# Kernel tuning notes

Hardware: AMD Instinct MI355X
Metric: run time of the kernel (lower is better)

The kernel has to match this reference:

```python
import jax, jax.numpy as jnp
import numpy as np

N_NODES = 50000
N_EDGES = 800000
IN_DIM = 128
HID = 128
NUM_GRAPHS = 64


def setup_inputs() -> dict:
    key = jax.random.key(0)
    ks = jax.random.split(key, 10)
    x = jax.random.normal(ks[0], (N_NODES, IN_DIM), dtype=jnp.float32)
    edge_index = jax.random.randint(ks[1], (2, N_EDGES), 0, N_NODES, dtype=jnp.int64)
    batch = jnp.sort(jax.random.randint(ks[2], (N_NODES,), 0, NUM_GRAPHS, dtype=jnp.int64))
    s = 1.0 / np.sqrt(IN_DIM)
    W0 = jax.random.uniform(ks[3], (IN_DIM, HID), jnp.float32, -s, s)
    b0 = jnp.zeros((HID,), jnp.float32)
    s = 1.0 / np.sqrt(HID)
    W1 = jax.random.uniform(ks[4], (HID, HID), jnp.float32, -s, s)
    b1 = jnp.zeros((HID,), jnp.float32)
    W2 = jax.random.uniform(ks[5], (HID, HID), jnp.float32, -s, s)
    b2 = jnp.zeros((HID,), jnp.float32)
    return {"x": x, "edge_index": edge_index, "batch": batch,
            "W0": W0, "b0": b0, "W1": W1, "b1": b1, "W2": W2, "b2": b2}


def reference(x, edge_index, batch, W0, b0, W1, b1, W2, b2):
    N = x.shape[0]
    # GCNConv: add self loops, symmetric degree normalization
    loop = jnp.arange(N, dtype=edge_index.dtype)
    src = jnp.concatenate([edge_index[0], loop])  # [E+N]
    dst = jnp.concatenate([edge_index[1], loop])
    deg = jax.ops.segment_sum(jnp.ones_like(dst, dtype=x.dtype), dst, num_segments=N)
    dinv = jnp.where(deg > 0, jax.lax.rsqrt(deg), 0.0)
    norm = (dinv[src] * dinv[dst])[:, None]  # [E+N, 1]

    def gcn_layer(h, W, b):
        h = h @ W  # [N, hid]
        agg = jax.ops.segment_sum(h[src] * norm, dst, num_segments=N)
        return agg + b

    h = jax.nn.relu(gcn_layer(x, W0, b0))
    h = jax.nn.relu(gcn_layer(h, W1, b1))
    h = jax.nn.relu(gcn_layer(h, W2, b2))
    # dropout is identity at inference (training=False)

    # global_mean_pool by batch index
    sums = jax.ops.segment_sum(h, batch, num_segments=NUM_GRAPHS)
    counts = jax.ops.segment_sum(jnp.ones((N,), h.dtype), batch, num_segments=NUM_GRAPHS)
    return sums / jnp.maximum(counts, 1.0)[:, None]
```

## Files before the change

kernel.cpp:

```cpp
#include <hip/hip_runtime.h>
#include <hip/hip_bf16.h>

#define NNODES 50000
#define NEDGES 800000
#define HIDDIM 128
#define NGRAPH 64
#define BUCKET 64

typedef __attribute__((ext_vector_type(8))) short short8;
typedef __attribute__((ext_vector_type(4))) float floatx4;

__device__ __forceinline__ float bfbits2f(unsigned short u) {
    return __uint_as_float(((unsigned int)u) << 16);
}
__device__ __forceinline__ unsigned short f2bfbits(float v) {
    __hip_bfloat16 h = __float2bfloat16(v);
    return __builtin_bit_cast(unsigned short, h);
}

__global__ void k_detect(const unsigned int* __restrict__ xw,
                         const unsigned int* __restrict__ eiw,
                         int* __restrict__ flags) {
    __shared__ int sh_hit, sh_zero;
    int t = threadIdx.x;
    if (t == 0) { sh_hit = 0; sh_zero = 0; }
    __syncthreads();
    if (t < 128) {
        unsigned int w = xw[t * 97 + 5];
        int e = (int)((w >> 7) & 0xFF);
        if (e >= 110 && e <= 140) atomicAdd(&sh_hit, 1);
        if (eiw[1001 + 2 * t] == 0) atomicAdd(&sh_zero, 1);
    }
    __syncthreads();
    if (t == 0) {
        flags[0] = (sh_hit >= 64) ? 1 : 0;
        flags[1] = (sh_zero >= 120) ? 1 : 0;
    }
}

__device__ __forceinline__ int ld_idx(const int* __restrict__ p, int j, int wide) {
    return wide ? p[2 * j] : p[j];
}

__global__ void k_zero_int(int* __restrict__ p, int n) {
    int i = blockIdx.x * 256 + threadIdx.x;
    if (i < n) p[i] = 0;
}

__global__ void k_append(const int* __restrict__ ei, const int* __restrict__ flags,
                         int* __restrict__ cnt, unsigned short* __restrict__ ecol) {
    int t = blockIdx.x * 256 + threadIdx.x;
    int e0 = t * 2;
    if (e0 >= NEDGES) return;
    int wide = flags[1];
    int s0, s1, d0, d1;
    if (wide) {
        int4 sv = ((const int4*)ei)[t];
        s0 = sv.x; s1 = sv.z;
        int4 dv = ((const int4*)(ei + 2 * NEDGES))[t];
        d0 = dv.x; d1 = dv.z;
    } else {
        int2 sv = ((const int2*)ei)[t];
        s0 = sv.x; s1 = sv.y;
        int2 dv = ((const int2*)(ei + NEDGES))[t];
        d0 = dv.x; d1 = dv.y;
    }
    int p0 = atomicAdd(&cnt[d0], 1);
    if (p0 < BUCKET) ecol[d0 * BUCKET + p0] = (unsigned short)s0;
    int p1 = atomicAdd(&cnt[d1], 1);
    if (p1 < BUCKET) ecol[d1 * BUCKET + p1] = (unsigned short)s1;
}

__global__ void k_dinv(const int* __restrict__ cnt, float* __restrict__ dinv) {
    int i = blockIdx.x * 256 + threadIdx.x;
    if (i < NNODES) dinv[i] = rsqrtf((float)cnt[i] + 1.0f);
}

__global__ __launch_bounds__(256) void k_gemm_mfma(const void* __restrict__ A,
                                                   const void* __restrict__ W,
                                                   const int* __restrict__ flags,
                                                   int a_mode,
                                                   const float* __restrict__ scale,
                                                   unsigned short* __restrict__ out,
                                                   int M) {
    __shared__ __align__(16) unsigned short Wl[16 * 128 * 8];
    __shared__ __align__(16) unsigned short Alds[64 * 17 * 8];
    const int tid = threadIdx.x;
    const int F = flags[0];
    const int abf = (a_mode == 2) ? 1 : (a_mode == 1 ? F : 0);
    const int row0 = blockIdx.x * 64;

    if (F) {
        const ushort4* __restrict__ Wg = (const ushort4*)W;
#pragma unroll
        for (int it = 0; it < 16; ++it) {
            int idx = it * 256 + tid;
            int k = idx >> 5, n = (idx & 31) * 4;
            ushort4 wv = Wg[idx];
            unsigned short* dst = &Wl[(((k >> 3) * 128) + n) * 8 + (k & 7)];
            dst[0] = wv.x; dst[8] = wv.y; dst[16] = wv.z; dst[24] = wv.w;
        }
    } else {
        const float4* __restrict__ Wg = (const float4*)W;
#pragma unroll
        for (int it = 0; it < 16; ++it) {
            int idx = it * 256 + tid;
            int k = idx >> 5, n = (idx & 31) * 4;
            float4 wv = Wg[idx];
            unsigned short* dst = &Wl[(((k >> 3) * 128) + n) * 8 + (k & 7)];
            dst[0] = f2bfbits(wv.x); dst[8]  = f2bfbits(wv.y);
            dst[16] = f2bfbits(wv.z); dst[24] = f2bfbits(wv.w);
        }
    }
    if (abf) {
#pragma unroll
        for (int it = 0; it < 4; ++it) {
            int idx = it * 256 + tid;
            int m = idx >> 4, kb = idx & 15;
            int gr = row0 + m;
            uint4 v = make_uint4(0, 0, 0, 0);
            if (gr < M) v = ((const uint4*)A)[(size_t)gr * 16 + kb];
            *reinterpret_cast<uint4*>(&Alds[(m * 17 + kb) * 8]) = v;
        }
    } else {
#pragma unroll
        for (int it = 0; it < 8; ++it) {
            int idx = it * 256 + tid;
            int m = idx >> 5, k4 = idx & 31;
            int k = k4 * 4;
            int gr = row0 + m;
            float4 v = make_float4(0, 0, 0, 0);
            if (gr < M) v = ((const float4*)A)[(size_t)gr * 32 + k4];
            ushort4 u;
            u.x = f2bfbits(v.x); u.y = f2bfbits(v.y);
            u.z = f2bfbits(v.z); u.w = f2bfbits(v.w);
            *reinterpret_cast<ushort4*>(&Alds[(m * 17 + (k >> 3)) * 8 + (k & 7)]) = u;
        }
    }
    __syncthreads();

    const int lane = tid & 63;
    const int wave = tid >> 6;
    const int q = lane >> 4;
    const int c = lane & 15;
    const int mrow = wave * 16 + c;
    floatx4 acc[8] = {};
#pragma unroll
    for (int k0 = 0; k0 < 4; ++k0) {
        int kb = k0 * 4 + q;
        short8 afrag = *reinterpret_cast<const short8*>(&Alds[(mrow * 17 + kb) * 8]);
#pragma unroll
        for (int t = 0; t < 8; ++t) {
            short8 bfrag = *reinterpret_cast<const short8*>(&Wl[(kb * 128 + t * 16 + c) * 8]);
            acc[t] = __builtin_amdgcn_mfma_f32_16x16x32_bf16(afrag, bfrag, acc[t], 0, 0, 0);
        }
    }
#pragma unroll
    for (int i = 0; i < 4; ++i) {
        int gr = row0 + wave * 16 + q * 4 + i;
        if (gr < M) {
            float s = scale ? scale[gr] : 1.0f;
#pragma unroll
            for (int t = 0; t < 8; ++t) {
                out[(size_t)gr * 128 + t * 16 + c] = f2bfbits(acc[t][i] * s);
            }
        }
    }
}

__global__ __launch_bounds__(256) void k_gather(const int* __restrict__ cnt,
                                                const unsigned short* __restrict__ ecol,
                                                const float* __restrict__ dinv,
                                                const unsigned short* __restrict__ tmp16,
                                                const void* __restrict__ bias,
                                                const int* __restrict__ flags,
                                                unsigned short* __restrict__ outh16) {
    int t = blockIdx.x * 256 + threadIdx.x;
    int n = t >> 5;
    if (n >= NNODES) return;
    int j = t & 31;
    int deg = cnt[n];
    if (deg > BUCKET) deg = BUCKET;
    const unsigned short* __restrict__ bk = &ecol[n * BUCKET];
    const ushort4* __restrict__ base = reinterpret_cast<const ushort4*>(tmp16);
    ushort4 u = base[(size_t)n * 32 + j];
    float ax = bfbits2f(u.x), ay = bfbits2f(u.y), az = bfbits2f(u.z), aw = bfbits2f(u.w);
    int k = 0;
    for (; k + 3 < deg; k += 4) {
        ushort4 sv = *reinterpret_cast<const ushort4*>(&bk[k]);
        int s0 = sv.x, s1 = sv.y, s2 = sv.z, s3 = sv.w;
        ushort4 u0 = base[(size_t)s0 * 32 + j];
        ushort4 u1 = base[(size_t)s1 * 32 + j];
        ushort4 u2 = base[(size_t)s2 * 32 + j];
        ushort4 u3 = base[(size_t)s3 * 32 + j];
        ax += (bfbits2f(u0.x) + bfbits2f(u1.x)) + (bfbits2f(u2.x) + bfbits2f(u3.x));
        ay += (bfbits2f(u0.y) + bfbits2f(u1.y)) + (bfbits2f(u2.y) + bfbits2f(u3.y));
        az += (bfbits2f(u0.z) + bfbits2f(u1.z)) + (bfbits2f(u2.z) + bfbits2f(u3.z));
        aw += (bfbits2f(u0.w) + bfbits2f(u1.w)) + (bfbits2f(u2.w) + bfbits2f(u3.w));
    }
    for (; k < deg; ++k) {
        ushort4 u0 = base[(size_t)bk[k] * 32 + j];
        ax += bfbits2f(u0.x); ay += bfbits2f(u0.y);
        az += bfbits2f(u0.z); aw += bfbits2f(u0.w);
    }
    float dn = dinv[n];
    ax *= dn; ay *= dn; az *= dn; aw *= dn;
    float b0, b1, b2, b3;
    if (flags[0]) {
        const unsigned short* bb = (const unsigned short*)bias;
        b0 = bfbits2f(bb[j * 4 + 0]); b1 = bfbits2f(bb[j * 4 + 1]);
        b2 = bfbits2f(bb[j * 4 + 2]); b3 = bfbits2f(bb[j * 4 + 3]);
    } else {
        const float* bb = (const float*)bias;
        b0 = bb[j * 4 + 0]; b1 = bb[j * 4 + 1]; b2 = bb[j * 4 + 2]; b3 = bb[j * 4 + 3];
    }
    ushort4 o;
    o.x = f2bfbits(fmaxf(ax + b0, 0.0f));
    o.y = f2bfbits(fmaxf(ay + b1, 0.0f));
    o.z = f2bfbits(fmaxf(az + b2, 0.0f));
    o.w = f2bfbits(fmaxf(aw + b3, 0.0f));
    reinterpret_cast<ushort4*>(outh16)[(size_t)n * 32 + j] = o;
}

__global__ __launch_bounds__(256) void k_gemm(const void* __restrict__ A,
                                              const void* __restrict__ W,
                                              const int* __restrict__ flags,
                                              int a_uses_flag,
                                              float* __restrict__ out, int M) {
    __shared__ __align__(16) float Al[32 * 128];
    const int tid = threadIdx.x;
    const int F = flags[0];
    const int afmt = a_uses_flag ? F : 0;
    const int row0 = blockIdx.x * 32;
#pragma unroll
    for (int j = 0; j < 16; ++j) {
        int idx = j * 256 + tid;
        int r = idx >> 7, k = idx & 127;
        int gr = row0 + r;
        float v = 0.0f;
        if (gr < M) {
            size_t off = (size_t)gr * 128 + k;
            v = afmt ? bfbits2f(((const unsigned short*)A)[off])
                     : ((const float*)A)[off];
        }
        Al[idx] = v;
    }
    __syncthreads();
    const int tx = tid & 31, ty = tid >> 5;
    const int c0 = tx * 4;
    float acc[4][4] = {};
    if (F) {
        const ushort4* __restrict__ Wg = (const ushort4*)W;
#pragma unroll 4
        for (int k = 0; k < 128; ++k) {
            ushort4 wv = Wg[k * 32 + tx];
            float w0 = bfbits2f(wv.x), w1 = bfbits2f(wv.y);
            float w2 = bfbits2f(wv.z), w3 = bfbits2f(wv.w);
#pragma unroll
            for (int i = 0; i < 4; ++i) {
                float a = Al[(ty + i * 8) * 128 + k];
                acc[i][0] = fmaf(a, w0, acc[i][0]);
                acc[i][1] = fmaf(a, w1, acc[i][1]);
                acc[i][2] = fmaf(a, w2, acc[i][2]);
                acc[i][3] = fmaf(a, w3, acc[i][3]);
            }
        }
    } else {
        const float4* __restrict__ Wg = (const float4*)W;
#pragma unroll 4
        for (int k = 0; k < 128; ++k) {
            float4 wv = Wg[k * 32 + tx];
#pragma unroll
            for (int i = 0; i < 4; ++i) {
                float a = Al[(ty + i * 8) * 128 + k];
                acc[i][0] = fmaf(a, wv.x, acc[i][0]);
                acc[i][1] = fmaf(a, wv.y, acc[i][1]);
                acc[i][2] = fmaf(a, wv.z, acc[i][2]);
                acc[i][3] = fmaf(a, wv.w, acc[i][3]);
            }
        }
    }
#pragma unroll
    for (int i = 0; i < 4; ++i) {
        int gr = row0 + ty + i * 8;
        if (gr < M) {
            *reinterpret_cast<float4*>(&out[(size_t)gr * 128 + c0]) =
                make_float4(acc[i][0], acc[i][1], acc[i][2], acc[i][3]);
        }
    }
}
__global__ void k_deg_init(float* __restrict__ deg) {
    int i = blockIdx.x * 256 + threadIdx.x;
    if (i < NNODES) deg[i] = 1.0f;
}
__global__ void k_deg_edges(const int* __restrict__ ei, const int* __restrict__ flags,
                            float* __restrict__ deg) {
    int e = blockIdx.x * 256 + threadIdx.x;
    if (e < NEDGES) unsafeAtomicAdd(&deg[ld_idx(ei, NEDGES + e, flags[1])], 1.0f);
}
__global__ void k_rsqrt(float* __restrict__ deg) {
    int i = blockIdx.x * 256 + threadIdx.x;
    if (i < NNODES) deg[i] = 1.0f / sqrtf(deg[i]);
}
__global__ void k_selfloop(const float* __restrict__ tmp, const float* __restrict__ dinv,
                           float* __restrict__ agg) {
    int t = blockIdx.x * 256 + threadIdx.x;
    if (t >= NNODES * 32) return;
    int n = t >> 5, j = t & 31;
    float s = dinv[n]; s = s * s;
    float4 v = *reinterpret_cast<const float4*>(&tmp[(size_t)n * 128 + j * 4]);
    v.x *= s; v.y *= s; v.z *= s; v.w *= s;
    *reinterpret_cast<float4*>(&agg[(size_t)n * 128 + j * 4]) = v;
}
__global__ __launch_bounds__(256) void k_scatter(const int* __restrict__ ei,
                                                 const int* __restrict__ flags,
                                                 const float* __restrict__ dinv,
                                                 const float* __restrict__ tmp,
                                                 float* __restrict__ agg) {
    int t = blockIdx.x * 256 + threadIdx.x;
    int e = t >> 5;
    if (e >= NEDGES) return;
    int j = t & 31;
    int wide = flags[1];
    int s = ld_idx(ei, e, wide);
    int d = ld_idx(ei, NEDGES + e, wide);
    float w = dinv[s] * dinv[d];
    const float4 v = *reinterpret_cast<const float4*>(&tmp[(size_t)s * 128 + j * 4]);
    float* p = &agg[(size_t)d * 128 + j * 4];
    unsafeAtomicAdd(p + 0, v.x * w);
    unsafeAtomicAdd(p + 1, v.y * w);
    unsafeAtomicAdd(p + 2, v.z * w);
    unsafeAtomicAdd(p + 3, v.w * w);
}
__global__ void k_bias_relu(float* __restrict__ h, const void* __restrict__ b,
                            const int* __restrict__ flags) {
    int t = blockIdx.x * 256 + threadIdx.x;
    if (t >= NNODES * 32) return;
    int j = t & 31;
    float b0, b1, b2, b3;
    if (flags[0]) {
        const unsigned short* bb = (const unsigned short*)b;
        b0 = bfbits2f(bb[j * 4 + 0]); b1 = bfbits2f(bb[j * 4 + 1]);
        b2 = bfbits2f(bb[j * 4 + 2]); b3 = bfbits2f(bb[j * 4 + 3]);
    } else {
        const float* bb = (const float*)b;
        b0 = bb[j * 4 + 0]; b1 = bb[j * 4 + 1]; b2 = bb[j * 4 + 2]; b3 = bb[j * 4 + 3];
    }
    float4 v = *reinterpret_cast<float4*>(&h[(size_t)t * 4]);
    v.x = fmaxf(v.x + b0, 0.0f);
    v.y = fmaxf(v.y + b1, 0.0f);
    v.z = fmaxf(v.z + b2, 0.0f);
    v.w = fmaxf(v.w + b3, 0.0f);
    *reinterpret_cast<float4*>(&h[(size_t)t * 4]) = v;
}

__global__ void k_bounds(const int* __restrict__ batch, const int* __restrict__ flags,
                         int* __restrict__ bounds) {
    int g = threadIdx.x;
    if (g > NGRAPH) return;
    int wide = flags[1];
    int lo = 0, hi = NNODES;
    while (lo < hi) {
        int mid = (lo + hi) >> 1;
        if (ld_idx(batch, mid, wide) < g) lo = mid + 1; else hi = mid;
    }
    bounds[g] = lo;
}

__global__ __launch_bounds__(256) void k_pool_part(const unsigned short* __restrict__ h16,
                                                   const int* __restrict__ bounds,
                                                   float* __restrict__ part) {
    __shared__ float sh[256 * 4];
    int g = blockIdx.x >> 2, seg = blockIdx.x & 3;
    int t = threadIdx.x;
    int c4 = t & 31, sub = t >> 5;
    int beg = bounds[g], end = bounds[g + 1];
    const ushort4* __restrict__ base = (const ushort4*)h16;
    float ax = 0, ay = 0, az = 0, aw = 0;
    for (int r = beg + seg * 8 + sub; r < end; r += 32) {
        ushort4 u = base[(size_t)r * 32 + c4];
        ax += bfbits2f(u.x); ay += bfbits2f(u.y);
        az += bfbits2f(u.z); aw += bfbits2f(u.w);
    }
    sh[t * 4 + 0] = ax; sh[t * 4 + 1] = ay; sh[t * 4 + 2] = az; sh[t * 4 + 3] = aw;
    __syncthreads();
    if (t < 32) {
        float4 r = make_float4(0, 0, 0, 0);
#pragma unroll
        for (int s = 0; s < 8; ++s) {
            r.x += sh[(s * 32 + t) * 4 + 0];
            r.y += sh[(s * 32 + t) * 4 + 1];
            r.z += sh[(s * 32 + t) * 4 + 2];
            r.w += sh[(s * 32 + t) * 4 + 3];
        }
        *reinterpret_cast<float4*>(&part[((size_t)(g * 4 + seg)) * 128 + t * 4]) = r;
    }
}

__global__ void k_pool_final(const float* __restrict__ part, const int* __restrict__ bounds,
                             const int* __restrict__ flags, void* __restrict__ out) {
    int i = blockIdx.x * 256 + threadIdx.x;
    if (i >= NGRAPH * 128) return;
    int g = i >> 7, col = i & 127;
    float s = part[(g * 4 + 0) * 128 + col] + part[(g * 4 + 1) * 128 + col] +
              part[(g * 4 + 2) * 128 + col] + part[(g * 4 + 3) * 128 + col];
    float c = (float)(bounds[g + 1] - bounds[g]);
    float r = s / fmaxf(c, 1.0f);
    if (flags[0]) ((__hip_bfloat16*)out)[i] = __float2bfloat16(r);
    else          ((float*)out)[i] = r;
}

__global__ __launch_bounds__(1024) void k_pool2(const float* __restrict__ h,
                                                const int* __restrict__ bounds,
                                                const int* __restrict__ flags,
                                                void* __restrict__ out) {
    __shared__ float sh[1024];
    int g = blockIdx.x;
    int t = threadIdx.x;
    int beg = bounds[g], end = bounds[g + 1];
    int col = t & 127, seg = t >> 7;
    float acc = 0.0f;
    for (int r = beg + seg; r < end; r += 8)
        acc += h[(size_t)r * 128 + col];
    sh[t] = acc;
    __syncthreads();
    if (t < 128) {
        float total = 0.0f;
#pragma unroll
        for (int i = 0; i < 8; ++i) total += sh[t + 128 * i];
        float c = (float)(end - beg);
        float r = total / fmaxf(c, 1.0f);
        if (flags[0]) ((__hip_bfloat16*)out)[g * 128 + t] = __float2bfloat16(r);
        else          ((float*)out)[g * 128 + t] = r;
    }
}

extern "C" void kernel_launch(void* const* d_in, const int* in_sizes, int n_in,
                              void* d_out, int out_size, void* d_ws, size_t ws_size,
                              hipStream_t stream) {
    const void* x  = d_in[0];
    const int* ei  = (const int*)d_in[1];
    const int* bat = (const int*)d_in[2];
    const void* W0 = d_in[3];
    const void* b0 = d_in[4];
    const void* W1 = d_in[5];
    const void* b1 = d_in[6];
    const void* W2 = d_in[7];
    const void* b2 = d_in[8];

    float* ws = (float*)d_ws;
    size_t off = 0;
    int*   flags  = (int*)ws;           off += 16;
    float* dinv   = ws + off;           off += 50176;
    float* hA     = ws + off;           off += (size_t)NNODES * 128;
    float* hB     = ws + off;           off += (size_t)NNODES * 128;
    int*   bounds = (int*)(ws + off);   off += 80;
    int*   cnt    = (int*)(ws + off);   off += 50304;
    float* part   = ws + off;           off += NGRAPH * 4 * 128 + 64;
    const size_t needed = off * 4;
    unsigned short* hA16 = (unsigned short*)hA;
    unsigned short* hB16 = (unsigned short*)hB;
    unsigned short* ecol = (unsigned short*)(hA + (size_t)NNODES * 64);

    const int bN  = (NNODES + 255) / 256;
    const int bE  = (NEDGES + 255) / 256;
    const int bNF = (NNODES * 32) / 256;
    const int bEF = (NEDGES * 32) / 256;
    const int bA  = (NEDGES / 2 + 255) / 256;
    const int bG  = (NNODES + 31) / 32;
    const int bG2 = (NNODES + 63) / 64;
    dim3 blk(256);

    hipLaunchKernelGGL(k_detect, dim3(1), blk, 0, stream,
                       (const unsigned int*)x, (const unsigned int*)ei, flags);

    const bool use_csr = (ws_size >= needed);

    if (use_csr) {
        hipLaunchKernelGGL(k_zero_int, dim3(bN), blk, 0, stream, cnt, 50176);
        hipLaunchKernelGGL(k_append, dim3(bA), blk, 0, stream, ei, flags, cnt, ecol);
        hipLaunchKernelGGL(k_dinv, dim3(bN), blk, 0, stream, cnt, dinv);

        hipLaunchKernelGGL(k_gemm_mfma, dim3(bG2), blk, 0, stream, x,    W0, flags, 1, dinv, hA16, NNODES);
        hipLaunchKernelGGL(k_gather,    dim3(bNF), blk, 0, stream, cnt, ecol, dinv, hA16, b0, flags, hB16);
        hipLaunchKernelGGL(k_gemm_mfma, dim3(bG2), blk, 0, stream, hB16, W1, flags, 2, dinv, hA16, NNODES);
        hipLaunchKernelGGL(k_gather,    dim3(bNF), blk, 0, stream, cnt, ecol, dinv, hA16, b1, flags, hB16);
        hipLaunchKernelGGL(k_gemm_mfma, dim3(bG2), blk, 0, stream, hB16, W2, flags, 2, dinv, hA16, NNODES);
        hipLaunchKernelGGL(k_gather,    dim3(bNF), blk, 0, stream, cnt, ecol, dinv, hA16, b2, flags, hB16);

        hipLaunchKernelGGL(k_bounds, dim3(1), dim3(128), 0, stream, bat, flags, bounds);
        hipLaunchKernelGGL(k_pool_part, dim3(NGRAPH * 4), blk, 0, stream, hB16, bounds, part);
        hipLaunchKernelGGL(k_pool_final, dim3(32), blk, 0, stream, part, bounds, flags, d_out);
    } else {
        hipLaunchKernelGGL(k_deg_init, dim3(bN), blk, 0, stream, dinv);
        hipLaunchKernelGGL(k_deg_edges, dim3(bE), blk, 0, stream, ei, flags, dinv);
        hipLaunchKernelGGL(k_rsqrt, dim3(bN), blk, 0, stream, dinv);

        hipLaunchKernelGGL(k_gemm, dim3(bG), blk, 0, stream, x, W0, flags, 1, hA, NNODES);
        hipLaunchKernelGGL(k_selfloop, dim3(bNF), blk, 0, stream, hA, dinv, hB);
        hipLaunchKernelGGL(k_scatter, dim3(bEF), blk, 0, stream, ei, flags, dinv, hA, hB);
        hipLaunchKernelGGL(k_bias_relu, dim3(bNF), blk, 0, stream, hB, b0, flags);

        hipLaunchKernelGGL(k_gemm, dim3(bG), blk, 0, stream, hB, W1, flags, 0, hA, NNODES);
        hipLaunchKernelGGL(k_selfloop, dim3(bNF), blk, 0, stream, hA, dinv, hB);
        hipLaunchKernelGGL(k_scatter, dim3(bEF), blk, 0, stream, ei, flags, dinv, hA, hB);
        hipLaunchKernelGGL(k_bias_relu, dim3(bNF), blk, 0, stream, hB, b1, flags);

        hipLaunchKernelGGL(k_gemm, dim3(bG), blk, 0, stream, hB, W2, flags, 0, hA, NNODES);
        hipLaunchKernelGGL(k_selfloop, dim3(bNF), blk, 0, stream, hA, dinv, hB);
        hipLaunchKernelGGL(k_scatter, dim3(bEF), blk, 0, stream, ei, flags, dinv, hA, hB);
        hipLaunchKernelGGL(k_bias_relu, dim3(bNF), blk, 0, stream, hB, b2, flags);

        hipLaunchKernelGGL(k_bounds, dim3(1), dim3(128), 0, stream, bat, flags, bounds);
        hipLaunchKernelGGL(k_pool2, dim3(NGRAPH), dim3(1024), 0, stream, hB, bounds, flags, d_out);
    }
}
```

Baseline: 335.9 us.

## Fuse gather aggregation into next layer GEMM and inline degree and bounds

Adds a k_fused kernel that gathers neighbor rows, applies normalization, bias and ReLU, stages the result in LDS, then runs the MFMA GEMM for the next layer. This removes two intermediate activation writes and reads plus two launches. The separate dinv and bounds kernels are also dropped, with rsqrt computed from counts inline and graph bounds found by binary search inside the pooling kernels. The cost is that each GEMM block now does the irregular gather work, which may lower occupancy or overlap relative to separate kernels.

Result: slower. 382.7 us (+13.9%).

```diff
diff --git a/kernel.cpp b/kernel.cpp
--- a/kernel.cpp
+++ b/kernel.cpp
@@ -40,6 +40,15 @@
 
 __device__ __forceinline__ int ld_idx(const int* __restrict__ p, int j, int wide) {
     return wide ? p[2 * j] : p[j];
+}
+
+__device__ __forceinline__ int find_bound(const int* __restrict__ batch, int wide, int g) {
+    int lo = 0, hi = NNODES;
+    while (lo < hi) {
+        int mid = (lo + hi) >> 1;
+        if (ld_idx(batch, mid, wide) < g) lo = mid + 1; else hi = mid;
+    }
+    return lo;
 }
 
 __global__ void k_zero_int(int* __restrict__ p, int n) {
@@ -71,16 +80,11 @@
     if (p1 < BUCKET) ecol[d1 * BUCKET + p1] = (unsigned short)s1;
 }
 
-__global__ void k_dinv(const int* __restrict__ cnt, float* __restrict__ dinv) {
-    int i = blockIdx.x * 256 + threadIdx.x;
-    if (i < NNODES) dinv[i] = rsqrtf((float)cnt[i] + 1.0f);
-}
-
 __global__ __launch_bounds__(256) void k_gemm_mfma(const void* __restrict__ A,
                                                    const void* __restrict__ W,
                                                    const int* __restrict__ flags,
                                                    int a_mode,
-                                                   const float* __restrict__ scale,
+                                                   const int* __restrict__ cntScale,
                                                    unsigned short* __restrict__ out,
                                                    int M) {
     __shared__ __align__(16) unsigned short Wl[16 * 128 * 8];
@@ -159,7 +163,7 @@
     for (int i = 0; i < 4; ++i) {
         int gr = row0 + wave * 16 + q * 4 + i;
         if (gr < M) {
-            float s = scale ? scale[gr] : 1.0f;
+            float s = cntScale ? rsqrtf((float)cntScale[gr] + 1.0f) : 1.0f;
 #pragma unroll
             for (int t = 0; t < 8; ++t) {
                 out[(size_t)gr * 128 + t * 16 + c] = f2bfbits(acc[t][i] * s);
@@ -168,9 +172,127 @@
     }
 }
 
+__global__ __launch_bounds__(256) void k_fused(const unsigned short* __restrict__ tmp16,
+                                               const void* __restrict__ W,
+                                               const int* __restrict__ flags,
+                                               const int* __restrict__ cnt,
+                                               const unsigned short* __restrict__ ecol,
+                                               const void* __restrict__ bias,
+                                               unsigned short* __restrict__ out,
+                                               int M) {
+    __shared__ __align__(16) unsigned short Wl[16 * 128 * 8];
+    __shared__ __align__(16) unsigned short Alds[64 * 17 * 8];
+    const int tid = threadIdx.x;
+    const int F = flags[0];
+    const int row0 = blockIdx.x * 64;
+
+    if (F) {
+        const ushort4* __restrict__ Wg = (const ushort4*)W;
+#pragma unroll
+        for (int it = 0; it < 16; ++it) {
+            int idx = it * 256 + tid;
+            int k = idx >> 5, n = (idx & 31) * 4;
+            ushort4 wv = Wg[idx];
+            unsigned short* dst = &Wl[(((k >> 3) * 128) + n) * 8 + (k & 7)];
+            dst[0] = wv.x; dst[8] = wv.y; dst[16] = wv.z; dst[24] = wv.w;
+        }
+    } else {
+        const float4* __restrict__ Wg = (const float4*)W;
+#pragma unroll
+        for (int it = 0; it < 16; ++it) {
+            int idx = it * 256 + tid;
+            int k = idx >> 5, n = (idx & 31) * 4;
+            float4 wv = Wg[idx];
+            unsigned short* dst = &Wl[(((k >> 3) * 128) + n) * 8 + (k & 7)];
+            dst[0] = f2bfbits(wv.x); dst[8]  = f2bfbits(wv.y);
+            dst[16] = f2bfbits(wv.z); dst[24] = f2bfbits(wv.w);
+        }
+    }
+
+    const int r8 = tid >> 5, j = tid & 31;
+    float b0, b1, b2, b3;
+    if (F) {
+        const unsigned short* bb = (const unsigned short*)bias;
+        b0 = bfbits2f(bb[j * 4 + 0]); b1 = bfbits2f(bb[j * 4 + 1]);
+        b2 = bfbits2f(bb[j * 4 + 2]); b3 = bfbits2f(bb[j * 4 + 3]);
+    } else {
+        const float* bb = (const float*)bias;
+        b0 = bb[j * 4 + 0]; b1 = bb[j * 4 + 1]; b2 = bb[j * 4 + 2]; b3 = bb[j * 4 + 3];
+    }
+    const ushort4* __restrict__ base = reinterpret_cast<const ushort4*>(tmp16);
+#pragma unroll
+    for (int it = 0; it < 8; ++it) {
+        int m = it * 8 + r8;
+        int n = row0 + m;
+        float ax = 0, ay = 0, az = 0, aw = 0;
+        if (n < M) {
+            int rawc = cnt[n];
+            int deg = rawc > BUCKET ? BUCKET : rawc;
+            ushort4 u = base[(size_t)n * 32 + j];
+            ax = bfbits2f(u.x); ay = bfbits2f(u.y);
+            az = bfbits2f(u.z); aw = bfbits2f(u.w);
+            const unsigned short* __restrict__ bk = &ecol[n * BUCKET];
+            int k = 0;
+            for (; k + 3 < deg; k += 4) {
+                ushort4 sv = *reinterpret_cast<const ushort4*>(&bk[k]);
+                ushort4 u0 = base[(size_t)sv.x * 32 + j];
+                ushort4 u1 = base[(size_t)sv.y * 32 + j];
+                ushort4 u2 = base[(size_t)sv.z * 32 + j];
+                ushort4 u3 = base[(size_t)sv.w * 32 + j];
+                ax += (bfbits2f(u0.x) + bfbits2f(u1.x)) + (bfbits2f(u2.x) + bfbits2f(u3.x));
+                ay += (bfbits2f(u0.y) + bfbits2f(u1.y)) + (bfbits2f(u2.y) + bfbits2f(u3.y));
+                az += (bfbits2f(u0.z) + bfbits2f(u1.z)) + (bfbits2f(u2.z) + bfbits2f(u3.z));
+                aw += (bfbits2f(u0.w) + bfbits2f(u1.w)) + (bfbits2f(u2.w) + bfbits2f(u3.w));
+            }
+            for (; k < deg; ++k) {
+                ushort4 u0 = base[(size_t)bk[k] * 32 + j];
+                ax += bfbits2f(u0.x); ay += bfbits2f(u0.y);
+                az += bfbits2f(u0.z); aw += bfbits2f(u0.w);
+            }
+            float dn = rsqrtf((float)rawc + 1.0f);
+            ax = fmaxf(ax * dn + b0, 0.0f);
+            ay = fmaxf(ay * dn + b1, 0.0f);
+            az = fmaxf(az * dn + b2, 0.0f);
+            aw = fmaxf(aw * dn + b3, 0.0f);
+        }
+        ushort4 o;
+        o.x = f2bfbits(ax); o.y = f2bfbits(ay);
+        o.z = f2bfbits(az); o.w = f2bfbits(aw);
+        *reinterpret_cast<ushort4*>(&Alds[(m * 17 + (j >> 1)) * 8 + (j & 1) * 4]) = o;
+    }
+    __syncthreads();
+
+    const int lane = tid & 63;
+    const int wave = tid >> 6;
+    const int q = lane >> 4;
+    const int c = lane & 15;
+    const int mrow = wave * 16 + c;
+    floatx4 acc[8] = {};
+#pragma unroll
+    for (int k0 = 0; k0 < 4; ++k0) {
+        int kb = k0 * 4 + q;
+        short8 afrag = *reinterpret_cast<const short8*>(&Alds[(mrow * 17 + kb) * 8]);
+#pragma unroll
+        for (int t = 0; t < 8; ++t) {
+            short8 bfrag = *reinterpret_cast<const short8*>(&Wl[(kb * 128 + t * 16 + c) * 8]);
+            acc[t] = __builtin_amdgcn_mfma_f32_16x16x32_bf16(afrag, bfrag, acc[t], 0, 0, 0);
+        }
+    }
+#pragma unroll
+    for (int i = 0; i < 4; ++i) {
+        int gr = row0 + wave * 16 + q * 4 + i;
+        if (gr < M) {
+            float s = rsqrtf((float)cnt[gr] + 1.0f);
+#pragma unroll
+            for (int t = 0; t < 8; ++t) {
+                out[(size_t)gr * 128 + t * 16 + c] = f2bfbits(acc[t][i] * s);
+            }
+        }
+    }
+}
+
 __global__ __launch_bounds__(256) void k_gather(const int* __restrict__ cnt,
                                                 const unsigned short* __restrict__ ecol,
-                                                const float* __restrict__ dinv,
                                                 const unsigned short* __restrict__ tmp16,
                                                 const void* __restrict__ bias,
                                                 const int* __restrict__ flags,
@@ -179,8 +301,8 @@
     int n = t >> 5;
     if (n >= NNODES) return;
     int j = t & 31;
-    int deg = cnt[n];
-    if (deg > BUCKET) deg = BUCKET;
+    int rawc = cnt[n];
+    int deg = rawc > BUCKET ? BUCKET : rawc;
     const unsigned short* __restrict__ bk = &ecol[n * BUCKET];
     const ushort4* __restrict__ base = reinterpret_cast<const ushort4*>(tmp16);
     ushort4 u = base[(size_t)n * 32 + j];
@@ -188,11 +310,10 @@
     int k = 0;
     for (; k + 3 < deg; k += 4) {
         ushort4 sv = *reinterpret_cast<const ushort4*>(&bk[k]);
-        int s0 = sv.x, s1 = sv.y, s2 = sv.z, s3 = sv.w;
-        ushort4 u0 = base[(size_t)s0 * 32 + j];
-        ushort4 u1 = base[(size_t)s1 * 32 + j];
-        ushort4 u2 = base[(size_t)s2 * 32 + j];
-        ushort4 u3 = base[(size_t)s3 * 32 + j];
+        ushort4 u0 = base[(size_t)sv.x * 32 + j];
+        ushort4 u1 = base[(size_t)sv.y * 32 + j];
+        ushort4 u2 = base[(size_t)sv.z * 32 + j];
+        ushort4 u3 = base[(size_t)sv.w * 32 + j];
         ax += (bfbits2f(u0.x) + bfbits2f(u1.x)) + (bfbits2f(u2.x) + bfbits2f(u3.x));
         ay += (bfbits2f(u0.y) + bfbits2f(u1.y)) + (bfbits2f(u2.y) + bfbits2f(u3.y));
         az += (bfbits2f(u0.z) + bfbits2f(u1.z)) + (bfbits2f(u2.z) + bfbits2f(u3.z));
@@ -203,7 +324,7 @@
         ax += bfbits2f(u0.x); ay += bfbits2f(u0.y);
         az += bfbits2f(u0.z); aw += bfbits2f(u0.w);
     }
-    float dn = dinv[n];
+    float dn = rsqrtf((float)rawc + 1.0f);
     ax *= dn; ay *= dn; az *= dn; aw *= dn;
     float b0, b1, b2, b3;
     if (flags[0]) {
@@ -354,27 +475,20 @@
     *reinterpret_cast<float4*>(&h[(size_t)t * 4]) = v;
 }
 
-__global__ void k_bounds(const int* __restrict__ batch, const int* __restrict__ flags,
-                         int* __restrict__ bounds) {
-    int g = threadIdx.x;
-    if (g > NGRAPH) return;
-    int wide = flags[1];
-    int lo = 0, hi = NNODES;
-    while (lo < hi) {
-        int mid = (lo + hi) >> 1;
-        if (ld_idx(batch, mid, wide) < g) lo = mid + 1; else hi = mid;
-    }
-    bounds[g] = lo;
-}
-
 __global__ __launch_bounds__(256) void k_pool_part(const unsigned short* __restrict__ h16,
-                                                   const int* __restrict__ bounds,
+                                                   const int* __restrict__ batch,
+                                                   const int* __restrict__ flags,
                                                    float* __restrict__ part) {
     __shared__ float sh[256 * 4];
+    __shared__ int sbeg, send;
     int g = blockIdx.x >> 2, seg = blockIdx.x & 3;
     int t = threadIdx.x;
+    int wide = flags[1];
+    if (t == 0) sbeg = find_bound(batch, wide, g);
+    if (t == 1) send = find_bound(batch, wide, g + 1);
+    __syncthreads();
+    int beg = sbeg, end = send;
     int c4 = t & 31, sub = t >> 5;
-    int beg = bounds[g], end = bounds[g + 1];
     const ushort4* __restrict__ base = (const ushort4*)h16;
     float ax = 0, ay = 0, az = 0, aw = 0;
     for (int r = beg + seg * 8 + sub; r < end; r += 32) {
@@ -397,27 +511,33 @@
     }
 }
 
-__global__ void k_pool_final(const float* __restrict__ part, const int* __restrict__ bounds,
+__global__ void k_pool_final(const float* __restrict__ part, const int* __restrict__ batch,
                              const int* __restrict__ flags, void* __restrict__ out) {
     int i = blockIdx.x * 256 + threadIdx.x;
     if (i >= NGRAPH * 128) return;
     int g = i >> 7, col = i & 127;
+    int wide = flags[1];
     float s = part[(g * 4 + 0) * 128 + col] + part[(g * 4 + 1) * 128 + col] +
               part[(g * 4 + 2) * 128 + col] + part[(g * 4 + 3) * 128 + col];
-    float c = (float)(bounds[g + 1] - bounds[g]);
+    float c = (float)(find_bound(batch, wide, g + 1) - find_bound(batch, wide, g));
     float r = s / fmaxf(c, 1.0f);
     if (flags[0]) ((__hip_bfloat16*)out)[i] = __float2bfloat16(r);
     else          ((float*)out)[i] = r;
 }
 
 __global__ __launch_bounds__(1024) void k_pool2(const float* __restrict__ h,
-                                                const int* __restrict__ bounds,
+                                                const int* __restrict__ batch,
                                                 const int* __restrict__ flags,
                                                 void* __restrict__ out) {
     __shared__ float sh[1024];
+    __shared__ int sbeg, send;
     int g = blockIdx.x;
     int t = threadIdx.x;
-    int beg = bounds[g], end = bounds[g + 1];
+    int wide = flags[1];
+    if (t == 0) sbeg = find_bound(batch, wide, g);
+    if (t == 1) send = find_bound(batch, wide, g + 1);
+    __syncthreads();
+    int beg = sbeg, end = send;
     int col = t & 127, seg = t >> 7;
     float acc = 0.0f;
     for (int r = beg + seg; r < end; r += 8)
@@ -454,7 +574,6 @@
     float* dinv   = ws + off;           off += 50176;
     float* hA     = ws + off;           off += (size_t)NNODES * 128;
     float* hB     = ws + off;           off += (size_t)NNODES * 128;
-    int*   bounds = (int*)(ws + off);   off += 80;
     int*   cnt    = (int*)(ws + off);   off += 50304;
     float* part   = ws + off;           off += NGRAPH * 4 * 128 + 64;
     const size_t needed = off * 4;
@@ -479,18 +598,14 @@
     if (use_csr) {
         hipLaunchKernelGGL(k_zero_int, dim3(bN), blk, 0, stream, cnt, 50176);
         hipLaunchKernelGGL(k_append, dim3(bA), blk, 0, stream, ei, flags, cnt, ecol);
-        hipLaunchKernelGGL(k_dinv, dim3(bN), blk, 0, stream, cnt, dinv);
-
-        hipLaunchKernelGGL(k_gemm_mfma, dim3(bG2), blk, 0, stream, x,    W0, flags, 1, dinv, hA16, NNODES);
-        hipLaunchKernelGGL(k_gather,    dim3(bNF), blk, 0, stream, cnt, ecol, dinv, hA16, b0, flags, hB16);
-        hipLaunchKernelGGL(k_gemm_mfma, dim3(bG2), blk, 0, stream, hB16, W1, flags, 2, dinv, hA16, NNODES);
-        hipLaunchKernelGGL(k_gather,    dim3(bNF), blk, 0, stream, cnt, ecol, dinv, hA16, b1, flags, hB16);
-        hipLaunchKernelGGL(k_gemm_mfma, dim3(bG2), blk, 0, stream, hB16, W2, flags, 2, dinv, hA16, NNODES);
-        hipLaunchKernelGGL(k_gather,    dim3(bNF), blk, 0, stream, cnt, ecol, dinv, hA16, b2, flags, hB16);
-
-        hipLaunchKernelGGL(k_bounds, dim3(1), dim3(128), 0, stream, bat, flags, bounds);
-        hipLaunchKernelGGL(k_pool_part, dim3(NGRAPH * 4), blk, 0, stream, hB16, bounds, part);
-        hipLaunchKernelGGL(k_pool_final, dim3(32), blk, 0, stream, part, bounds, flags, d_out);
+
+        hipLaunchKernelGGL(k_gemm_mfma, dim3(bG2), blk, 0, stream, x, W0, flags, 1, cnt, hA16, NNODES);
+        hipLaunchKernelGGL(k_fused, dim3(bG2), blk, 0, stream, hA16, W1, flags, cnt, ecol, b0, hB16, NNODES);
+        hipLaunchKernelGGL(k_fused, dim3(bG2), blk, 0, stream, hB16, W2, flags, cnt, ecol, b1, hA16, NNODES);
+        hipLaunchKernelGGL(k_gather, dim3(bNF), blk, 0, stream, cnt, ecol, hA16, b2, flags, hB16);
+
+        hipLaunchKernelGGL(k_pool_part, dim3(NGRAPH * 4), blk, 0, stream, hB16, bat, flags, part);
+        hipLaunchKernelGGL(k_pool_final, dim3(32), blk, 0, stream, part, bat, flags, d_out);
     } else {
         hipLaunchKernelGGL(k_deg_init, dim3(bN), blk, 0, stream, dinv);
         hipLaunchKernelGGL(k_deg_edges, dim3(bE), blk, 0, stream, ei, flags, dinv);
@@ -511,7 +626,6 @@
         hipLaunchKernelGGL(k_scatter, dim3(bEF), blk, 0, stream, ei, flags, dinv, hA, hB);
         hipLaunchKernelGGL(k_bias_relu, dim3(bNF), blk, 0, stream, hB, b2, flags);
 
-        hipLaunchKernelGGL(k_bounds, dim3(1), dim3(128), 0, stream, bat, flags, bounds);
-        hipLaunchKernelGGL(k_pool2, dim3(NGRAPH), dim3(1024), 0, stream, hB, bounds, flags, d_out);
-    }
-}
+        hipLaunchKernelGGL(k_pool2, dim3(NGRAPH), dim3(1024), 0, stream, hB, bat, flags, d_out);
+    }
+}
```
